# Kernel tuning notes

Measured on AMD Instinct MI355X. Metric: run time of the kernel, lower is better.

The kernel has to match this reference:

```python
import jax, jax.numpy as jnp
import numpy as np

N_MEL = 80; ARNN = 1024; ADIM = 128; EMB = 512; PRE = 256; DRNN = 1024; NF = 32; KS = 31
B = 32; NCTX = 512; T = 500
PAD = (KS - 1) // 2


def setup_inputs() -> dict:
    key = jax.random.key(0)
    ks = jax.random.split(key, 20)
    g = lambda k, shape: jax.random.normal(k, shape, dtype=jnp.float32) * 0.02
    return {
        "memory": jax.random.normal(ks[0], (B, NCTX, EMB), dtype=jnp.float32),
        "decoder_inputs": jax.random.normal(ks[1], (B, N_MEL, T), dtype=jnp.float32),
        "mask": jnp.zeros((B, NCTX), dtype=bool),
        "prenet_w1": g(ks[2], (PRE, N_MEL)),
        "prenet_w2": g(ks[3], (PRE, PRE)),
        "arnn_wih": g(ks[4], (4 * ARNN, PRE + EMB)),
        "arnn_whh": g(ks[5], (4 * ARNN, ARNN)),
        "arnn_bih": jnp.zeros((4 * ARNN,), jnp.float32),
        "arnn_bhh": jnp.zeros((4 * ARNN,), jnp.float32),
        "q_w": g(ks[6], (ADIM, ARNN)),
        "m_w": g(ks[7], (ADIM, EMB)),
        "loc_conv_w": g(ks[8], (NF, 2, KS)),
        "loc_w": g(ks[9], (ADIM, NF)),
        "v_w": g(ks[10], (ADIM,)),
        "drnn_wih": g(ks[11], (4 * DRNN, ARNN + EMB)),
        "drnn_whh": g(ks[12], (4 * DRNN, DRNN)),
        "drnn_bih": jnp.zeros((4 * DRNN,), jnp.float32),
        "drnn_bhh": jnp.zeros((4 * DRNN,), jnp.float32),
        "proj_w": g(ks[13], (N_MEL, DRNN + EMB)),
        "proj_b": jnp.zeros((N_MEL,), jnp.float32),
        "gate_w": g(ks[14], (1, DRNN + EMB)),
        "gate_b": jnp.zeros((1,), jnp.float32),
    }


def _lstm_cell(x, h, c, wih, whh, bih, bhh):
    # PyTorch LSTMCell gate order: i, f, g, o
    z = x @ wih.T + h @ whh.T + bih + bhh
    i, f, g, o = jnp.split(z, 4, axis=-1)
    c2 = jax.nn.sigmoid(f) * c + jax.nn.sigmoid(i) * jnp.tanh(g)
    h2 = jax.nn.sigmoid(o) * jnp.tanh(c2)
    return h2, c2


def reference(memory, decoder_inputs, mask,
              prenet_w1, prenet_w2,
              arnn_wih, arnn_whh, arnn_bih, arnn_bhh,
              q_w, m_w, loc_conv_w, loc_w, v_w,
              drnn_wih, drnn_whh, drnn_bih, drnn_bhh,
              proj_w, proj_b, gate_w, gate_b):
    b, n_ctx, emb = memory.shape
    n_mel, t_out = decoder_inputs.shape[1], decoder_inputs.shape[2]

    # (time, batch, n_mel) with a leading zero go-frame; PreNet (eval: no dropout)
    x = jnp.transpose(decoder_inputs, (2, 0, 1))
    x = jnp.concatenate([jnp.zeros((1, b, n_mel), x.dtype), x], axis=0)
    h = jax.nn.relu(x @ prenet_w1.T)
    h = jax.nn.relu(h @ prenet_w2.T)  # (T+1, B, PRE)
    inputs = h[:-1]  # T decoder steps

    proc_mem = memory @ m_w.T  # (B, n_ctx, ADIM)

    def step(carry, xin):
        ah, ac, dh, dc, aw, awc, actx = carry
        cell_in = jnp.concatenate([xin, actx], axis=-1)
        ah, ac = _lstm_cell(cell_in, ah, ac, arnn_wih, arnn_whh, arnn_bih, arnn_bhh)
        # location-sensitive attention
        aw_cat = jnp.stack([aw, awc], axis=1)  # (B, 2, n_ctx)
        loc = jax.lax.conv_general_dilated(
            aw_cat, loc_conv_w, window_strides=(1,), padding=[(PAD, PAD)],
            dimension_numbers=("NCH", "OIH", "NCH"))  # (B, NF, n_ctx)
        loc = jnp.transpose(loc, (0, 2, 1)) @ loc_w.T  # (B, n_ctx, ADIM)
        q = (ah @ q_w.T)[:, None, :]  # (B, 1, ADIM)
        e = jnp.tanh(q + proc_mem + loc) @ v_w  # (B, n_ctx)
        e = jnp.where(mask, -1e9, e)
        aw = jax.nn.softmax(e, axis=-1)
        actx = jnp.einsum("bn,bne->be", aw, memory)
        awc = awc + aw
        din = jnp.concatenate([ah, actx], axis=-1)
        dh, dc = _lstm_cell(din, dh, dc, drnn_wih, drnn_whh, drnn_bih, drnn_bhh)
        dhc = jnp.concatenate([dh, actx], axis=-1)
        mel = dhc @ proj_w.T + proj_b  # (B, n_mel)
        gate = dhc @ gate_w.T + gate_b  # (B, 1)
        return (ah, ac, dh, dc, aw, awc, actx), (mel, gate[:, 0])

    z32 = lambda *s: jnp.zeros(s, memory.dtype)
    carry0 = (z32(b, ARNN), z32(b, ARNN), z32(b, DRNN), z32(b, DRNN),
              z32(b, n_ctx), z32(b, n_ctx), z32(b, emb))
    _, (mels, gates) = jax.lax.scan(step, carry0, inputs)
    mel_out = jnp.transpose(mels, (1, 2, 0))   # (B, n_mel, T)
    gate_out = jnp.transpose(gates, (1, 0))    # (B, T)
    return mel_out, gate_out
```

## Files before the change

### kernel.cpp

```cpp
#include <hip/hip_runtime.h>

#define NBLK 256
#define NTHR 512

constexpr int kNMel = 80, kArnn = 1024, kAdim = 128, kEmb = 512, kPre = 256;
constexpr int kNF = 32, kKS = 31, kB = 32, kNctx = 512, kT = 500, kPad = 15;

constexpr int KT_A = 56;
constexpr int KT_D = 80;
constexpr int KT_ALL = KT_A + KT_D;

constexpr int OFF_PREB   = 0;
constexpr int OFF_PROCMB = OFF_PREB + kT * kB * kPre / 2;
constexpr int OFF_QWTB   = OFF_PROCMB + kB * kNctx * kAdim / 2;
constexpr int OFF_LWT    = OFF_QWTB + kAdim * kArnn / 2;
constexpr int OFF_STATE  = OFF_LWT + kAdim * 33;
constexpr int OFF_AHB    = OFF_STATE;
constexpr int OFF_DHB    = OFF_AHB + 2 * kB * kArnn / 2;
constexpr int OFF_DH     = OFF_DHB + 2 * kB * kArnn / 2;
constexpr int OFF_AC     = OFF_DH + 2 * kB * kArnn;
constexpr int OFF_DC     = OFF_AC + kB * kArnn;
constexpr int OFF_ACTX   = OFF_DC + kB * kArnn;
constexpr int OFF_AW     = OFF_ACTX + kB * kEmb;
constexpr int OFF_AWC    = OFF_AW + kB * kNctx;
constexpr int OFF_PAW    = OFF_AWC + kB * kNctx;
constexpr int OFF_NUM    = OFF_PAW + kB * kNctx;
constexpr int OFF_DEN    = OFF_NUM + 2 * kB * kEmb;
constexpr int OFF_END    = OFF_DEN + 2 * kB;
constexpr int STATE_SZ   = OFF_END - OFF_STATE;
constexpr int OFF_BAR    = OFF_END;
constexpr int BAR_LINES  = 266;
constexpr int OFF_PAN    = OFF_BAR + BAR_LINES * 32;
constexpr int PAN_SZ     = NBLK * KT_ALL * 256;
constexpr int OFF_GMB    = OFF_PAN + PAN_SZ;
constexpr int GMB_SZ     = kB * kNctx * kEmb / 2;

typedef __attribute__((ext_vector_type(4))) float fvec4;
typedef __attribute__((ext_vector_type(8))) short bh8_t;
typedef unsigned long long u64;
typedef unsigned short ushortt;

union U64u { u64 u; float2 f2; ushortt s[4]; };

union SMem {
  struct { ushortt xs[8][2][2048]; } x1;
  struct { float zra[4][2][64][4]; float zrd[4][2][64][4];
           float hb[2][32][4]; } x2;
  struct { float ahb_s[kArnn]; float vw_s[kAdim]; float psum[512]; float q_s[kAdim];
           float aw_s[96]; float awc_s[96]; float cw[kNF * 2 * kKS];
           float loc_s[64 * 33]; float p_s[64]; float lwt[kAdim * 33];
           float dhc[kArnn + kEmb]; float pprj[126];
           ushortt pm[64 * kAdim]; } b;
  struct { float x8[8][80]; float h1[8][256]; } p;
  struct { float mem_s[4][512]; } m;
};

__device__ __forceinline__ float sigf(float x) { return 1.0f / (1.0f + __expf(-x)); }
__device__ __forceinline__ float tanhfast(float x) { return 1.0f - 2.0f / (__expf(2.0f * x) + 1.0f); }

__device__ __forceinline__ ushortt bf16rn(float f) {
  unsigned u = __float_as_uint(f);
  unsigned r = (u + 0x7FFFu + ((u >> 16) & 1u)) >> 16;
  return (ushortt)r;
}
__device__ __forceinline__ float bf2f(ushortt v) {
  return __uint_as_float((unsigned)v << 16);
}

__device__ __forceinline__ u64 ald64(const void* p) {
  return __hip_atomic_load((const u64*)p, __ATOMIC_RELAXED, __HIP_MEMORY_SCOPE_AGENT);
}
__device__ __forceinline__ float alf(const float* p) {
  return __hip_atomic_load(p, __ATOMIC_RELAXED, __HIP_MEMORY_SCOPE_AGENT);
}
__device__ __forceinline__ void asf(float* p, float v) {
  __hip_atomic_store(p, v, __ATOMIC_RELAXED, __HIP_MEMORY_SCOPE_AGENT);
}
__device__ __forceinline__ void as64(void* p, u64 v) {
  __hip_atomic_store((u64*)p, v, __ATOMIC_RELAXED, __HIP_MEMORY_SCOPE_AGENT);
}
__device__ __forceinline__ unsigned alu(const unsigned* p) {
  return __hip_atomic_load(p, __ATOMIC_RELAXED, __HIP_MEMORY_SCOPE_AGENT);
}
__device__ __forceinline__ void asu(unsigned* p, unsigned v) {
  __hip_atomic_store(p, v, __ATOMIC_RELAXED, __HIP_MEMORY_SCOPE_AGENT);
}

__device__ __forceinline__ void gbar_full(unsigned* cnt, unsigned* gen, unsigned& genv) {
  __syncthreads();
  if (threadIdx.x == 0) {
    __threadfence();
    unsigned arrived = __hip_atomic_fetch_add(cnt, 1u, __ATOMIC_ACQ_REL, __HIP_MEMORY_SCOPE_AGENT) + 1u;
    if (arrived == (unsigned)NBLK) {
      __hip_atomic_store(cnt, 0u, __ATOMIC_RELAXED, __HIP_MEMORY_SCOPE_AGENT);
      __hip_atomic_fetch_add(gen, 1u, __ATOMIC_ACQ_REL, __HIP_MEMORY_SCOPE_AGENT);
    } else {
      while (__hip_atomic_load(gen, __ATOMIC_ACQUIRE, __HIP_MEMORY_SCOPE_AGENT) == genv) {
        __builtin_amdgcn_s_sleep(2);
      }
    }
    ++genv;
  }
  __syncthreads();
}

__device__ __forceinline__ void gbar_light(unsigned* bar, unsigned target, int bk, int tid) {
  asm volatile("s_waitcnt vmcnt(0) lgkmcnt(0)" ::: "memory");
  __syncthreads();
  if (bk == 0) {
    if (tid < 64) {
      if (tid == 0) {
        asm volatile("s_waitcnt vmcnt(0)" ::: "memory");
      }
      unsigned i1 = (unsigned)tid * 4 + 1, i2 = i1 + 1, i3 = i1 + 2;
      unsigned i0 = (unsigned)tid * 4;
      for (;;) {
        bool ok = true;
        if (i0 != 0) ok = ok && (alu(&bar[i0 * 32]) >= target);
        ok = ok && (alu(&bar[i1 * 32]) >= target);
        ok = ok && (alu(&bar[i2 * 32]) >= target);
        ok = ok && (alu(&bar[i3 * 32]) >= target);
        if (__all(ok)) break;
        __builtin_amdgcn_s_sleep(1);
      }
      if (tid < 8) asu(&bar[(256 + tid) * 32], target);
    }
  } else {
    if (tid == 0) {
      asm volatile("s_waitcnt vmcnt(0)" ::: "memory");
      asu(&bar[bk * 32], target);
      unsigned* wk = &bar[(256 + (bk & 7)) * 32];
      while (alu(wk) < target) __builtin_amdgcn_s_sleep(1);
    }
  }
  __syncthreads();
}

template<int LS, int W>
__device__ __forceinline__ void lstm_wave(
    const ushortt* __restrict__ s0, const ushortt* __restrict__ s2,
    const float* __restrict__ numq, const float* __restrict__ invden,
    const short* __restrict__ pan,
    int l, ushortt* xstg, fvec4& z0, fvec4& z1)
{
  constexpr int NC  = LS ? 10 : 7;
  constexpr int CB  = LS ? W * 640 : W * 448;
  constexpr int KT0 = LS ? W * 20 : W * 14;
  constexpr int BD0 = LS ? 1024 : 256;
  constexpr int BD1 = LS ? 1536 : 768;
  const int u8 = l & 15, rj = l >> 4;
  const int m = l & 15, kg = l >> 4;

  u64 L0[8], L1[8];
  bh8_t f00, f01, f10, f11;

  auto load = [&](int c, u64* L, bh8_t& f0, bh8_t& f1) {
    const int c0 = CB + c * 64;
    if (c0 >= BD0 && c0 < BD1) {
      const float* base = numq + (c0 - BD0) + u8 * 4;
      #pragma unroll
      for (int j = 0; j < 8; ++j) {
        int row = 4 * j + rj;
        const float* fp = base + (size_t)row * kEmb;
        U64u a, b2; a.u = ald64(fp); b2.u = ald64(fp + 2);
        float s = invden[row];
        U64u pk;
        pk.s[0] = bf16rn(a.f2.x * s);  pk.s[1] = bf16rn(a.f2.y * s);
        pk.s[2] = bf16rn(b2.f2.x * s); pk.s[3] = bf16rn(b2.f2.y * s);
        L[j] = pk.u;
      }
    } else {
      const ushortt* bsrc; int stride; bool coh;
      if (c0 < BD0) { bsrc = s0 + c0;       stride = (LS ? 1024 : 256); coh = (LS == 1); }
      else          { bsrc = s2 + c0 - BD1; stride = 1024;              coh = true; }
      #pragma unroll
      for (int j = 0; j < 8; ++j) {
        const ushortt* ap = bsrc + (size_t)(4 * j + rj) * stride + u8 * 4;
        L[j] = coh ? ald64(ap) : *reinterpret_cast<const u64*>(ap);
      }
    }
    f0 = *reinterpret_cast<const bh8_t*>(pan + (size_t)(KT0 + c * 2) * 512 + l * 8);
    f1 = *reinterpret_cast<const bh8_t*>(pan + (size_t)(KT0 + c * 2 + 1) * 512 + l * 8);
  };
  auto stash = [&](int buf, u64* L) {
    #pragma unroll
    for (int j = 0; j < 8; ++j) {
      int row = 4 * j + rj;
      int sw = u8 ^ ((row & 7) << 1);
      *reinterpret_cast<u64*>(xstg + buf * 2048 + row * 64 + sw * 4) = L[j];
    }
  };
  auto consume = [&](int buf, bh8_t f0, bh8_t f1) {
    #pragma unroll
    for (int kt = 0; kt < 2; ++kt) {
      int sw = (2 * (kt * 4 + kg)) ^ ((m & 7) << 1);
      bh8_t a0 = *reinterpret_cast<const bh8_t*>(xstg + buf * 2048 + m * 64 + sw * 4);
      bh8_t a1 = *reinterpret_cast<const bh8_t*>(xstg + buf * 2048 + (16 + m) * 64 + sw * 4);
      bh8_t f = kt ? f1 : f0;
      z0 = __builtin_amdgcn_mfma_f32_16x16x32_bf16(a0, f, z0, 0, 0, 0);
      z1 = __builtin_amdgcn_mfma_f32_16x16x32_bf16(a1, f, z1, 0, 0, 0);
    }
  };

  load(0, L0, f00, f01);
  #pragma unroll
  for (int c = 0; c < NC; c += 2) {
    stash(0, L0);
    if (c + 1 < NC) load(c + 1, L1, f10, f11);
    consume(0, f00, f01);
    if (c + 1 < NC) {
      stash(1, L1);
      if (c + 2 < NC) load(c + 2, L0, f00, f01);
      consume(1, f10, f11);
    }
  }
}

extern "C" __global__ void __launch_bounds__(NTHR, 1)
decoder_kernel(const float* __restrict__ gmem, const float* __restrict__ dec,
               const unsigned char* __restrict__ mask,
               const float* __restrict__ pw1, const float* __restrict__ pw2,
               const float* __restrict__ awih, const float* __restrict__ awhh,
               const float* __restrict__ abih, const float* __restrict__ abhh,
               const float* __restrict__ qw, const float* __restrict__ mw,
               const float* __restrict__ cvw, const float* __restrict__ locw,
               const float* __restrict__ vw,
               const float* __restrict__ dwih, const float* __restrict__ dwhh,
               const float* __restrict__ dbih, const float* __restrict__ dbhh,
               const float* __restrict__ pjw, const float* __restrict__ pjb,
               const float* __restrict__ gw, const float* __restrict__ gb,
               float* __restrict__ out, float* __restrict__ ws, int useg)
{
  __shared__ SMem sm;
  __shared__ float s_invden[32];
  const int bk = blockIdx.x, tid = threadIdx.x;
  unsigned genv_f = 0, bcnt = 0;
  unsigned* bar = reinterpret_cast<unsigned*>(ws + OFF_BAR);
  unsigned* cntF = &bar[264 * 32];
  unsigned* genF = &bar[265 * 32];

  ushortt* PREBu = reinterpret_cast<ushortt*>(ws + OFF_PREB);
  ushortt* PROCMBu = reinterpret_cast<ushortt*>(ws + OFF_PROCMB);
  ushortt* QWTBu = reinterpret_cast<ushortt*>(ws + OFF_QWTB);
  float* LWT = ws + OFF_LWT;
  ushortt* AHBu = reinterpret_cast<ushortt*>(ws + OFF_AHB);
  ushortt* DHBu = reinterpret_cast<ushortt*>(ws + OFF_DHB);
  float* DH = ws + OFF_DH;
  float* AC = ws + OFF_AC;
  float* DC = ws + OFF_DC;
  float* ACTX = ws + OFF_ACTX;
  float* AWp = ws + OFF_AW;
  float* AWC = ws + OFF_AWC;
  float* PAW = ws + OFF_PAW;
  float* NUM = ws + OFF_NUM;
  float* DEN = ws + OFF_DEN;
  short* PANS = reinterpret_cast<short*>(ws + OFF_PAN);
  ushortt* GMB = reinterpret_cast<ushortt*>(ws + OFF_GMB);

  for (int i = bk * NTHR + tid; i < STATE_SZ; i += NBLK * NTHR) (ws + OFF_STATE)[i] = 0.f;
  for (int i = bk * NTHR + tid; i < kAdim * kArnn; i += NBLK * NTHR)
    QWTBu[i] = bf16rn(qw[i]);
  for (int i = bk * NTHR + tid; i < kAdim * kNF; i += NBLK * NTHR) {
    int d = i >> 5, f = i & 31;
    LWT[d * 33 + f] = locw[i];
  }
  gbar_full(cntF, genF, genv_f);

  if (bk == 0 && tid < 2 * kB) asf(&DEN[tid], 1.0f);
  for (int it = 0; it < 16; ++it) {
    int task0 = bk * 64 + it * 4;
    for (int i = tid; i < 2048; i += NTHR) {
      int pr = i >> 9, h = i & 511;
      sm.m.mem_s[pr][h] = gmem[(size_t)(task0 + pr) * kEmb + h];
    }
    __syncthreads();
    {
      int pr = tid >> 7, d = tid & 127;
      const float* mwr = mw + d * kEmb;
      float acc = 0.f;
      for (int h = 0; h < kEmb; ++h) acc = fmaf(sm.m.mem_s[pr][h], mwr[h], acc);
      PROCMBu[(size_t)(task0 + pr) * kAdim + d] = bf16rn(acc);
    }
    if (useg) {
      for (int i = tid; i < 2048; i += NTHR) {
        int pr = i >> 9, h = i & 511;
        GMB[(size_t)(task0 + pr) * kEmb + h] = bf16rn(sm.m.mem_s[pr][h]);
      }
    }
    __syncthreads();
  }
  for (int g = bk; g < 2000; g += NBLK) {
    int t_idx = g >> 2;
    int b0 = (g & 3) * 8;
    if (t_idx == 0) {
      for (int i = tid; i < 8 * kPre; i += NTHR)
        PREBu[(size_t)(b0 + (i >> 8)) * kPre + (i & 255)] = 0;
      continue;
    }
    for (int i = tid; i < 640; i += NTHR) {
      int bb = i / 80, m2 = i % 80;
      sm.p.x8[bb][m2] = dec[((size_t)(b0 + bb) * kNMel + m2) * kT + (t_idx - 1)];
    }
    __syncthreads();
    {
      int u = tid & 255, rep = tid >> 8;
      float acc[4] = {0.f, 0.f, 0.f, 0.f};
      for (int m2 = 0; m2 < 80; ++m2) {
        float w = pw1[u * kNMel + m2];
        #pragma unroll
        for (int r = 0; r < 4; ++r) acc[r] = fmaf(w, sm.p.x8[rep * 4 + r][m2], acc[r]);
      }
      #pragma unroll
      for (int r = 0; r < 4; ++r) sm.p.h1[rep * 4 + r][u] = fmaxf(acc[r], 0.f);
    }
    __syncthreads();
    {
      int u = tid & 255, rep = tid >> 8;
      float acc[4] = {0.f, 0.f, 0.f, 0.f};
      for (int k = 0; k < kPre; ++k) {
        float w = pw2[u * kPre + k];
        #pragma unroll
        for (int r = 0; r < 4; ++r) acc[r] = fmaf(w, sm.p.h1[rep * 4 + r][k], acc[r]);
      }
      #pragma unroll
      for (int r = 0; r < 4; ++r)
        PREBu[((size_t)t_idx * kB + b0 + rep * 4 + r) * kPre + u] = bf16rn(fmaxf(acc[r], 0.f));
    }
    __syncthreads();
  }
  {
    const int UNITS = NBLK * KT_ALL * 64;
    for (int u = bk * NTHR + tid; u < UNITS; u += NBLK * NTHR) {
      int bkk = u / (KT_ALL * 64);
      int rem = u - bkk * (KT_ALL * 64);
      int kta = rem >> 6, l = rem & 63;
      int lstm = (kta >= KT_A);
      int kt = lstm ? kta - KT_A : kta;
      int n = l & 15, kg = l >> 4;
      int r = (n >> 2) * 1024 + bkk * 4 + (n & 3);
      bh8_t v;
      #pragma unroll
      for (int j = 0; j < 8; ++j) {
        int k = kt * 32 + kg * 8 + j;
        float wv;
        if (!lstm) wv = (k < 768) ? awih[(size_t)r * 768 + k] : awhh[(size_t)r * 1024 + (k - 768)];
        else       wv = (k < 1536) ? dwih[(size_t)r * 1536 + k] : dwhh[(size_t)r * 1024 + (k - 1536)];
        v[j] = (short)bf16rn(wv);
      }
      *reinterpret_cast<bh8_t*>(PANS + (size_t)u * 8) = v;
    }
  }
  gbar_full(cntF, genF, genv_f);

  for (int t = 0; t <= kT; ++t) {
    const int p = t & 1, q = p ^ 1;
    float* nump = NUM + p * kB * kEmb;
    const float* numq = NUM + q * kB * kEmb;

    if (tid < kB) s_invden[tid] = 1.0f / alf(DEN + q * kB + tid);
    __syncthreads();
    if (t > 0 && tid < 64) {
      int idx = bk * 64 + tid;
      int b2 = idx >> 9;
      float invd = s_invden[b2];
      float av = PAW[idx] * invd;
      asf(&AWp[idx], av);
      asf(&AWC[idx], alf(&AWC[idx]) + av);
      asf(&ACTX[idx], alf(&numq[idx]) * invd);
    }
    if (t < kT) {
      if (tid < 64) asf(&nump[bk * 64 + tid], 0.f);
      if (bk == 0 && tid < kB) asf(DEN + p * kB + tid, 0.f);
    }
    {
      const int w8 = tid >> 6, l = tid & 63;
      fvec4 z0 = {0.f, 0.f, 0.f, 0.f}, z1 = z0;
      const ushortt* AHBq_ = AHBu + q * kB * kArnn;
      const ushortt* DHBp_ = DHBu + p * kB * kArnn;
      const ushortt* preb_t = PREBu + (size_t)t * kB * kPre;
      ushortt* xst = &sm.x1.xs[w8][0][0];
      const short* panb = PANS + (size_t)bk * (KT_ALL * 512);
      const short* pand = panb + KT_A * 512;
      if (w8 < 4) {
        if (t < kT) {
          switch (w8) {
            case 0: lstm_wave<0,0>(preb_t, AHBq_, numq, s_invden, panb, l, xst, z0, z1); break;
            case 1: lstm_wave<0,1>(preb_t, AHBq_, numq, s_invden, panb, l, xst, z0, z1); break;
            case 2: lstm_wave<0,2>(preb_t, AHBq_, numq, s_invden, panb, l, xst, z0, z1); break;
            default: lstm_wave<0,3>(preb_t, AHBq_, numq, s_invden, panb, l, xst, z0, z1); break;
          }
        }
      } else {
        if (t > 0) {
          switch (w8) {
            case 4: lstm_wave<1,0>(AHBq_, DHBp_, numq, s_invden, pand, l, xst, z0, z1); break;
            case 5: lstm_wave<1,1>(AHBq_, DHBp_, numq, s_invden, pand, l, xst, z0, z1); break;
            case 6: lstm_wave<1,2>(AHBq_, DHBp_, numq, s_invden, pand, l, xst, z0, z1); break;
            default: lstm_wave<1,3>(AHBq_, DHBp_, numq, s_invden, pand, l, xst, z0, z1); break;
          }
        }
      }
      __syncthreads();
      if (w8 < 4) {
        *reinterpret_cast<fvec4*>(&sm.x2.zra[w8][0][l][0]) = z0;
        *reinterpret_cast<fvec4*>(&sm.x2.zra[w8][1][l][0]) = z1;
      } else {
        *reinterpret_cast<fvec4*>(&sm.x2.zrd[w8 - 4][0][l][0]) = z0;
        *reinterpret_cast<fvec4*>(&sm.x2.zrd[w8 - 4][1][l][0]) = z1;
      }
    }
    __syncthreads();
    if (tid < 256) {
      const int ls = tid >> 7, uu = (tid >> 5) & 3, b = tid & 31;
      const bool go = (ls == 0) ? (t < kT) : (t > 0);
      if (go) {
        const int mt = b >> 4, mm = b & 15;
        const int lane_base = (mm >> 2) * 16, rr = mm & 3;
        float zg[4];
        #pragma unroll
        for (int g = 0; g < 4; ++g) {
          int ln = lane_base + g * 4 + uu;
          float s;
          if (ls == 0)
            s = sm.x2.zra[0][mt][ln][rr] + sm.x2.zra[1][mt][ln][rr]
              + sm.x2.zra[2][mt][ln][rr] + sm.x2.zra[3][mt][ln][rr];
          else
            s = sm.x2.zrd[0][mt][ln][rr] + sm.x2.zrd[1][mt][ln][rr]
              + sm.x2.zrd[2][mt][ln][rr] + sm.x2.zrd[3][mt][ln][rr];
          int rg = g * 1024 + bk * 4 + uu;
          s += (ls ? dbih[rg] + dbhh[rg] : abih[rg] + abhh[rg]);
          zg[g] = s;
        }
        float* cst = ls ? DC : AC;
        const int idx = b * kArnn + bk * 4 + uu;
        float c = sigf(zg[1]) * cst[idx] + sigf(zg[0]) * tanhfast(zg[2]);
        cst[idx] = c;
        float h = sigf(zg[3]) * tanhfast(c);
        if (ls) asf(&DH[q * kB * kArnn + idx], h);
        sm.x2.hb[ls][b][uu] = h;
      }
    }
    __syncthreads();
    if (tid < 64) {
      int ls = tid >> 5, b = tid & 31;
      bool go2 = ls ? (t > 0) : (t < kT);
      if (go2) {
        U64u pk;
        #pragma unroll
        for (int j = 0; j < 4; ++j) pk.s[j] = bf16rn(sm.x2.hb[ls][b][j]);
        ushortt* dst = (ls ? (DHBu + q * kB * kArnn) : (AHBu + p * kB * kArnn)) + b * kArnn + bk * 4;
        as64(dst, pk.u);
      }
    }
    gbar_light(bar, ++bcnt, bk, tid);

    if (t < kT) {
      const int b = bk >> 3, sub = bk & 7, j0 = sub * 64;
      const int pbase = (sub == 0) ? 0 : 21 + (sub - 1) * 20;
      const int pcnt = (sub == 0) ? 21 : 20;
      const ushortt* AHBp_ = AHBu + p * kB * kArnn;
      if (tid < 256) {
        U64u v; v.u = ald64(AHBp_ + b * kArnn + tid * 4);
        #pragma unroll
        for (int j = 0; j < 4; ++j) sm.b.ahb_s[tid * 4 + j] = bf2f(v.s[j]);
      }
      for (int i = tid; i < 94; i += NTHR) {
        int jj = j0 - kPad + i;
        bool ok = (jj >= 0 && jj < kNctx);
        sm.b.aw_s[i] = ok ? alf(&AWp[b * kNctx + jj]) : 0.f;
        sm.b.awc_s[i] = ok ? alf(&AWC[b * kNctx + jj]) : 0.f;
      }
      for (int i = tid; i < kNF * 2 * kKS; i += NTHR) sm.b.cw[i] = cvw[i];
      for (int i = tid; i < kAdim * 33; i += NTHR) sm.b.lwt[i] = LWT[i];
      for (int i = tid; i < kAdim; i += NTHR) sm.b.vw_s[i] = vw[i];
      {
        const fvec4* src = reinterpret_cast<const fvec4*>(PROCMBu + (size_t)(b * kNctx + j0) * kAdim);
        fvec4* dst = reinterpret_cast<fvec4*>(sm.b.pm);
        for (int i = tid; i < 1024; i += NTHR) dst[i] = src[i];
      }
      if (sub < 4 && t > 0) {
        for (int i = tid; i < kArnn + kEmb; i += NTHR)
          sm.b.dhc[i] = (i < kArnn) ? alf(&DH[q * kB * kArnn + b * kArnn + i])
                                    : alf(&ACTX[b * kEmb + (i - kArnn)]);
      }
      __syncthreads();
      {
        int d = tid & 127, qr = tid >> 7;
        const ushortt* wq = QWTBu + (size_t)d * kArnn + qr * 256;
        const float* ahs = sm.b.ahb_s + qr * 256;
        float acc = 0.f;
        #pragma unroll 4
        for (int h8 = 0; h8 < 32; ++h8) {
          U64u a, c2;
          a.u = *reinterpret_cast<const u64*>(wq + h8 * 8);
          c2.u = *reinterpret_cast<const u64*>(wq + h8 * 8 + 4);
          #pragma unroll
          for (int j = 0; j < 4; ++j) acc = fmaf(bf2f(a.s[j]), ahs[h8 * 8 + j], acc);
          #pragma unroll
          for (int j = 0; j < 4; ++j) acc = fmaf(bf2f(c2.s[j]), ahs[h8 * 8 + 4 + j], acc);
        }
        sm.b.psum[tid] = acc;
      }
      __syncthreads();
      if (tid < kAdim)
        sm.b.q_s[tid] = sm.b.psum[tid] + sm.b.psum[128 + tid]
                      + sm.b.psum[256 + tid] + sm.b.psum[384 + tid];
      {
        int j = tid >> 3, f0 = (tid & 7) * 4;
        #pragma unroll
        for (int fi = 0; fi < 4; ++fi) {
          int f = f0 + fi;
          const float* w0 = &sm.b.cw[f * 62];
          float s = 0.f;
          for (int k = 0; k < kKS; ++k)
            s = fmaf(sm.b.aw_s[j + k], w0[k], fmaf(sm.b.awc_s[j + k], w0[31 + k], s));
          sm.b.loc_s[j * 33 + f] = s;
        }
      }
      if (sub < 4 && t > 0 && tid < pcnt * 6) {
        int ol = tid / 6, kc = tid % 6, og = pbase + ol;
        const float* row = (og < kNMel) ? pjw + (size_t)og * (kArnn + kEmb) : gw;
        const float* x = sm.b.dhc + kc * 256;
        const float* r2 = row + kc * 256;
        float acc = 0.f;
        for (int k = 0; k < 256; ++k) acc = fmaf(r2[k], x[k], acc);
        sm.b.pprj[tid] = acc;
      }
      __syncthreads();
      {
        int j = tid >> 3, grp = tid & 7, jj = j0 + j;
        float pe = 0.f;
        #pragma unroll 4
        for (int dd = 0; dd < 16; ++dd) {
          int d = grp + 8 * dd;
          float l2 = 0.f;
          const float* ls2 = &sm.b.loc_s[j * 33];
          const float* lw2 = &sm.b.lwt[d * 33];
          #pragma unroll 8
          for (int f = 0; f < kNF; ++f) l2 = fmaf(ls2[f], lw2[f], l2);
          float x = sm.b.q_s[d] + bf2f(sm.b.pm[j * kAdim + d]) + l2;
          pe = fmaf(sm.b.vw_s[d], tanhfast(x), pe);
        }
        pe += __shfl_xor(pe, 1);
        pe += __shfl_xor(pe, 2);
        pe += __shfl_xor(pe, 4);
        if (grp == 0) {
          float pv = mask[b * kNctx + jj] ? 0.f : __expf(pe);
          sm.b.p_s[j] = pv;
          PAW[b * kNctx + jj] = pv;
        }
      }
      if (sub < 4 && t > 0 && tid < pcnt) {
        int og = pbase + tid;
        float val = (og < kNMel) ? pjb[og] : gb[0];
        #pragma unroll
        for (int kc = 0; kc < 6; ++kc) val += sm.b.pprj[tid * 6 + kc];
        if (og < kNMel) out[((size_t)b * kNMel + og) * kT + (t - 1)] = val;
        else out[(size_t)kB * kNMel * kT + b * kT + (t - 1)] = val;
      }
      __syncthreads();
      if (tid < 64) {
        float v = sm.b.p_s[tid];
        #pragma unroll
        for (int o = 1; o < 64; o <<= 1) v += __shfl_xor(v, o);
        if (tid == 0) atomicAdd(DEN + p * kB + b, v);
      }
      if (useg) {
        const ushortt* memb = GMB + (size_t)(b * kNctx + j0) * kEmb + tid;
        float a0 = 0.f, a1 = 0.f, a2 = 0.f, a3 = 0.f;
        #pragma unroll 4
        for (int jj2 = 0; jj2 < 64; jj2 += 4) {
          a0 = fmaf(sm.b.p_s[jj2],     bf2f(memb[(size_t)jj2 * kEmb]), a0);
          a1 = fmaf(sm.b.p_s[jj2 + 1], bf2f(memb[(size_t)(jj2 + 1) * kEmb]), a1);
          a2 = fmaf(sm.b.p_s[jj2 + 2], bf2f(memb[(size_t)(jj2 + 2) * kEmb]), a2);
          a3 = fmaf(sm.b.p_s[jj2 + 3], bf2f(memb[(size_t)(jj2 + 3) * kEmb]), a3);
        }
        atomicAdd(&nump[b * kEmb + tid], (a0 + a1) + (a2 + a3));
      } else {
        const float* memb = gmem + (size_t)(b * kNctx + j0) * kEmb + tid;
        float a0 = 0.f, a1 = 0.f;
        #pragma unroll 8
        for (int jj2 = 0; jj2 < 64; jj2 += 2) {
          a0 = fmaf(sm.b.p_s[jj2], memb[(size_t)jj2 * kEmb], a0);
          a1 = fmaf(sm.b.p_s[jj2 + 1], memb[(size_t)(jj2 + 1) * kEmb], a1);
        }
        atomicAdd(&nump[b * kEmb + tid], a0 + a1);
      }
      gbar_light(bar, ++bcnt, bk, tid);
    }
  }

  if (bk < kB) {
    const int b = bk;
    for (int i = tid; i < kArnn + kEmb; i += NTHR)
      sm.b.dhc[i] = (i < kArnn) ? alf(&DH[1 * kB * kArnn + b * kArnn + i])
                                : alf(&ACTX[b * kEmb + (i - kArnn)]);
    __syncthreads();
    if (tid < 486) {
      int ol = tid / 6, kc = tid % 6;
      const float* row = (ol < kNMel) ? pjw + (size_t)ol * (kArnn + kEmb) : gw;
      const float* x = sm.b.dhc + kc * 256;
      const float* r2 = row + kc * 256;
      float acc = 0.f;
      for (int k = 0; k < 256; ++k) acc = fmaf(r2[k], x[k], acc);
      sm.b.psum[tid] = acc;
    }
    __syncthreads();
    if (tid < 81) {
      float val = (tid < kNMel) ? pjb[tid] : gb[0];
      #pragma unroll
      for (int kc = 0; kc < 6; ++kc) val += sm.b.psum[tid * 6 + kc];
      if (tid < kNMel) out[((size_t)b * kNMel + tid) * kT + (kT - 1)] = val;
      else out[(size_t)kB * kNMel * kT + b * kT + (kT - 1)] = val;
    }
  }
}

extern "C" void kernel_launch(void* const* d_in, const int* in_sizes, int n_in,
                              void* d_out, int out_size, void* d_ws, size_t ws_size,
                              hipStream_t stream) {
  const float* gmem = (const float*)d_in[0];
  const float* dec = (const float*)d_in[1];
  const unsigned char* mask = (const unsigned char*)d_in[2];
  const float* pw1 = (const float*)d_in[3];
  const float* pw2 = (const float*)d_in[4];
  const float* awih = (const float*)d_in[5];
  const float* awhh = (const float*)d_in[6];
  const float* abih = (const float*)d_in[7];
  const float* abhh = (const float*)d_in[8];
  const float* qw = (const float*)d_in[9];
  const float* mw = (const float*)d_in[10];
  const float* cvw = (const float*)d_in[11];
  const float* locw = (const float*)d_in[12];
  const float* vw = (const float*)d_in[13];
  const float* dwih = (const float*)d_in[14];
  const float* dwhh = (const float*)d_in[15];
  const float* dbih = (const float*)d_in[16];
  const float* dbhh = (const float*)d_in[17];
  const float* pjw = (const float*)d_in[18];
  const float* pjb = (const float*)d_in[19];
  const float* gw = (const float*)d_in[20];
  const float* gb = (const float*)d_in[21];
  float* out = (float*)d_out;
  float* ws = (float*)d_ws;

  int useg = (ws_size >= (size_t)(OFF_GMB + GMB_SZ) * sizeof(float)) ? 1 : 0;

  hipMemsetAsync((char*)d_ws + (size_t)OFF_BAR * sizeof(float), 0,
                 (size_t)BAR_LINES * 128, stream);
  hipLaunchKernelGGL(decoder_kernel, dim3(NBLK), dim3(NTHR), 0, stream,
                     gmem, dec, mask, pw1, pw2, awih, awhh, abih, abhh, qw, mw,
                     cvw, locw, vw, dwih, dwhh, dbih, dbhh, pjw, pjb, gw, gb,
                     out, ws, useg);
}
```

Baseline: 38.91 ms.

## Double block size to 1024 threads and split LSTM waves by M-half

Raises threads per block from 512 to 1024 and splits each LSTM GEMM slice across two waves, with each wave owning one 16-row half of the batch and a single MFMA accumulator instead of two. The query projection reduction and the attention-context accumulation over memory rows are also split across the extra threads, and some phases are gated to the first 512 threads. The intent is more latency hiding and shorter per-wave serial chains within each persistent step. In exchange it adds register pressure limits (launch bounds changed to 1024,4), duplicated fragment loads of the weight panels, and more atomics to the context accumulator.

```diff
diff --git a/kernel.cpp b/kernel.cpp
--- a/kernel.cpp
+++ b/kernel.cpp
@@ -1,7 +1,7 @@
 #include <hip/hip_runtime.h>
 
 #define NBLK 256
-#define NTHR 512
+#define NTHR 1024
 
 constexpr int kNMel = 80, kArnn = 1024, kAdim = 128, kEmb = 512, kPre = 256;
 constexpr int kNF = 32, kKS = 31, kB = 32, kNctx = 512, kT = 500, kPad = 15;
@@ -43,10 +43,10 @@
 union U64u { u64 u; float2 f2; ushortt s[4]; };
 
 union SMem {
-  struct { ushortt xs[8][2][2048]; } x1;
+  struct { ushortt xs[16][2048]; } x1;
   struct { float zra[4][2][64][4]; float zrd[4][2][64][4];
            float hb[2][32][4]; } x2;
-  struct { float ahb_s[kArnn]; float vw_s[kAdim]; float psum[512]; float q_s[kAdim];
+  struct { float ahb_s[kArnn]; float vw_s[kAdim]; float psum[1024]; float q_s[kAdim];
            float aw_s[96]; float awc_s[96]; float cw[kNF * 2 * kKS];
            float loc_s[64 * 33]; float p_s[64]; float lwt[kAdim * 33];
            float dhc[kArnn + kEmb]; float pprj[126];
@@ -109,11 +109,8 @@
   __syncthreads();
   if (bk == 0) {
     if (tid < 64) {
-      if (tid == 0) {
-        asm volatile("s_waitcnt vmcnt(0)" ::: "memory");
-      }
-      unsigned i1 = (unsigned)tid * 4 + 1, i2 = i1 + 1, i3 = i1 + 2;
-      unsigned i0 = (unsigned)tid * 4;
+      if (tid == 0) asm volatile("s_waitcnt vmcnt(0)" ::: "memory");
+      unsigned i0 = (unsigned)tid * 4, i1 = i0 + 1, i2 = i0 + 2, i3 = i0 + 3;
       for (;;) {
         bool ok = true;
         if (i0 != 0) ok = ok && (alu(&bar[i0 * 32]) >= target);
@@ -136,22 +133,22 @@
   __syncthreads();
 }
 
-template<int LS, int W>
+template<int LS, int SL, int MH>
 __device__ __forceinline__ void lstm_wave(
     const ushortt* __restrict__ s0, const ushortt* __restrict__ s2,
     const float* __restrict__ numq, const float* __restrict__ invden,
     const short* __restrict__ pan,
-    int l, ushortt* xstg, fvec4& z0, fvec4& z1)
+    int l, ushortt* xs, fvec4& z)
 {
   constexpr int NC  = LS ? 10 : 7;
-  constexpr int CB  = LS ? W * 640 : W * 448;
-  constexpr int KT0 = LS ? W * 20 : W * 14;
+  constexpr int CB  = LS ? SL * 640 : SL * 448;
+  constexpr int KT0 = LS ? SL * 20 : SL * 14;
   constexpr int BD0 = LS ? 1024 : 256;
   constexpr int BD1 = LS ? 1536 : 768;
   const int u8 = l & 15, rj = l >> 4;
   const int m = l & 15, kg = l >> 4;
 
-  u64 L0[8], L1[8];
+  u64 L0[4], L1[4];
   bh8_t f00, f01, f10, f11;
 
   auto load = [&](int c, u64* L, bh8_t& f0, bh8_t& f1) {
@@ -159,11 +156,11 @@
     if (c0 >= BD0 && c0 < BD1) {
       const float* base = numq + (c0 - BD0) + u8 * 4;
       #pragma unroll
-      for (int j = 0; j < 8; ++j) {
-        int row = 4 * j + rj;
-        const float* fp = base + (size_t)row * kEmb;
+      for (int j = 0; j < 4; ++j) {
+        int lr = 4 * j + rj;
+        const float* fp = base + (size_t)(MH * 16 + lr) * kEmb;
         U64u a, b2; a.u = ald64(fp); b2.u = ald64(fp + 2);
-        float s = invden[row];
+        float s = invden[MH * 16 + lr];
         U64u pk;
         pk.s[0] = bf16rn(a.f2.x * s);  pk.s[1] = bf16rn(a.f2.y * s);
         pk.s[2] = bf16rn(b2.f2.x * s); pk.s[3] = bf16rn(b2.f2.y * s);
@@ -174,8 +171,8 @@
       if (c0 < BD0) { bsrc = s0 + c0;       stride = (LS ? 1024 : 256); coh = (LS == 1); }
       else          { bsrc = s2 + c0 - BD1; stride = 1024;              coh = true; }
       #pragma unroll
-      for (int j = 0; j < 8; ++j) {
-        const ushortt* ap = bsrc + (size_t)(4 * j + rj) * stride + u8 * 4;
+      for (int j = 0; j < 4; ++j) {
+        const ushortt* ap = bsrc + (size_t)(MH * 16 + 4 * j + rj) * stride + u8 * 4;
         L[j] = coh ? ald64(ap) : *reinterpret_cast<const u64*>(ap);
       }
     }
@@ -184,21 +181,18 @@
   };
   auto stash = [&](int buf, u64* L) {
     #pragma unroll
-    for (int j = 0; j < 8; ++j) {
-      int row = 4 * j + rj;
-      int sw = u8 ^ ((row & 7) << 1);
-      *reinterpret_cast<u64*>(xstg + buf * 2048 + row * 64 + sw * 4) = L[j];
+    for (int j = 0; j < 4; ++j) {
+      int lr = 4 * j + rj;
+      int sw = u8 ^ ((lr & 7) << 1);
+      *reinterpret_cast<u64*>(xs + buf * 1024 + lr * 64 + sw * 4) = L[j];
     }
   };
   auto consume = [&](int buf, bh8_t f0, bh8_t f1) {
     #pragma unroll
     for (int kt = 0; kt < 2; ++kt) {
       int sw = (2 * (kt * 4 + kg)) ^ ((m & 7) << 1);
-      bh8_t a0 = *reinterpret_cast<const bh8_t*>(xstg + buf * 2048 + m * 64 + sw * 4);
-      bh8_t a1 = *reinterpret_cast<const bh8_t*>(xstg + buf * 2048 + (16 + m) * 64 + sw * 4);
-      bh8_t f = kt ? f1 : f0;
-      z0 = __builtin_amdgcn_mfma_f32_16x16x32_bf16(a0, f, z0, 0, 0, 0);
-      z1 = __builtin_amdgcn_mfma_f32_16x16x32_bf16(a1, f, z1, 0, 0, 0);
+      bh8_t a = *reinterpret_cast<const bh8_t*>(xs + buf * 1024 + m * 64 + sw * 4);
+      z = __builtin_amdgcn_mfma_f32_16x16x32_bf16(a, kt ? f1 : f0, z, 0, 0, 0);
     }
   };
 
@@ -216,7 +210,7 @@
   }
 }
 
-extern "C" __global__ void __launch_bounds__(NTHR, 1)
+extern "C" __global__ void __launch_bounds__(NTHR, 4)
 decoder_kernel(const float* __restrict__ gmem, const float* __restrict__ dec,
                const unsigned char* __restrict__ mask,
                const float* __restrict__ pw1, const float* __restrict__ pw2,
@@ -274,7 +268,7 @@
       sm.m.mem_s[pr][h] = gmem[(size_t)(task0 + pr) * kEmb + h];
     }
     __syncthreads();
-    {
+    if (tid < 512) {
       int pr = tid >> 7, d = tid & 127;
       const float* mwr = mw + d * kEmb;
       float acc = 0.f;
@@ -302,7 +296,7 @@
       sm.p.x8[bb][m2] = dec[((size_t)(b0 + bb) * kNMel + m2) * kT + (t_idx - 1)];
     }
     __syncthreads();
-    {
+    if (tid < 512) {
       int u = tid & 255, rep = tid >> 8;
       float acc[4] = {0.f, 0.f, 0.f, 0.f};
       for (int m2 = 0; m2 < 80; ++m2) {
@@ -314,7 +308,7 @@
       for (int r = 0; r < 4; ++r) sm.p.h1[rep * 4 + r][u] = fmaxf(acc[r], 0.f);
     }
     __syncthreads();
-    {
+    if (tid < 512) {
       int u = tid & 255, rep = tid >> 8;
       float acc[4] = {0.f, 0.f, 0.f, 0.f};
       for (int k = 0; k < kPre; ++k) {
@@ -373,41 +367,45 @@
       if (bk == 0 && tid < kB) asf(DEN + p * kB + tid, 0.f);
     }
     {
-      const int w8 = tid >> 6, l = tid & 63;
-      fvec4 z0 = {0.f, 0.f, 0.f, 0.f}, z1 = z0;
+      const int wid = tid >> 6, l = tid & 63;
+      fvec4 z = {0.f, 0.f, 0.f, 0.f};
       const ushortt* AHBq_ = AHBu + q * kB * kArnn;
       const ushortt* DHBp_ = DHBu + p * kB * kArnn;
       const ushortt* preb_t = PREBu + (size_t)t * kB * kPre;
-      ushortt* xst = &sm.x1.xs[w8][0][0];
+      ushortt* xs = &sm.x1.xs[wid][0];
       const short* panb = PANS + (size_t)bk * (KT_ALL * 512);
       const short* pand = panb + KT_A * 512;
-      if (w8 < 4) {
+      if (wid < 8) {
         if (t < kT) {
-          switch (w8) {
-            case 0: lstm_wave<0,0>(preb_t, AHBq_, numq, s_invden, panb, l, xst, z0, z1); break;
-            case 1: lstm_wave<0,1>(preb_t, AHBq_, numq, s_invden, panb, l, xst, z0, z1); break;
-            case 2: lstm_wave<0,2>(preb_t, AHBq_, numq, s_invden, panb, l, xst, z0, z1); break;
-            default: lstm_wave<0,3>(preb_t, AHBq_, numq, s_invden, panb, l, xst, z0, z1); break;
+          switch (wid) {
+            case 0: lstm_wave<0,0,0>(preb_t, AHBq_, numq, s_invden, panb, l, xs, z); break;
+            case 1: lstm_wave<0,0,1>(preb_t, AHBq_, numq, s_invden, panb, l, xs, z); break;
+            case 2: lstm_wave<0,1,0>(preb_t, AHBq_, numq, s_invden, panb, l, xs, z); break;
+            case 3: lstm_wave<0,1,1>(preb_t, AHBq_, numq, s_invden, panb, l, xs, z); break;
+            case 4: lstm_wave<0,2,0>(preb_t, AHBq_, numq, s_invden, panb, l, xs, z); break;
+            case 5: lstm_wave<0,2,1>(preb_t, AHBq_, numq, s_invden, panb, l, xs, z); break;
+            case 6: lstm_wave<0,3,0>(preb_t, AHBq_, numq, s_invden, panb, l, xs, z); break;
+            default: lstm_wave<0,3,1>(preb_t, AHBq_, numq, s_invden, panb, l, xs, z); break;
           }
         }
       } else {
         if (t > 0) {
-          switch (w8) {
-            case 4: lstm_wave<1,0>(AHBq_, DHBp_, numq, s_invden, pand, l, xst, z0, z1); break;
-            case 5: lstm_wave<1,1>(AHBq_, DHBp_, numq, s_invden, pand, l, xst, z0, z1); break;
-            case 6: lstm_wave<1,2>(AHBq_, DHBp_, numq, s_invden, pand, l, xst, z0, z1); break;
-            default: lstm_wave<1,3>(AHBq_, DHBp_, numq, s_invden, pand, l, xst, z0, z1); break;
+          switch (wid) {
+            case 8:  lstm_wave<1,0,0>(AHBq_, DHBp_, numq, s_invden, pand, l, xs, z); break;
+            case 9:  lstm_wave<1,0,1>(AHBq_, DHBp_, numq, s_invden, pand, l, xs, z); break;
+            case 10: lstm_wave<1,1,0>(AHBq_, DHBp_, numq, s_invden, pand, l, xs, z); break;
+            case 11: lstm_wave<1,1,1>(AHBq_, DHBp_, numq, s_invden, pand, l, xs, z); break;
+            case 12: lstm_wave<1,2,0>(AHBq_, DHBp_, numq, s_invden, pand, l, xs, z); break;
+            case 13: lstm_wave<1,2,1>(AHBq_, DHBp_, numq, s_invden, pand, l, xs, z); break;
+            case 14: lstm_wave<1,3,0>(AHBq_, DHBp_, numq, s_invden, pand, l, xs, z); break;
+            default: lstm_wave<1,3,1>(AHBq_, DHBp_, numq, s_invden, pand, l, xs, z); break;
           }
         }
       }
       __syncthreads();
-      if (w8 < 4) {
-        *reinterpret_cast<fvec4*>(&sm.x2.zra[w8][0][l][0]) = z0;
-        *reinterpret_cast<fvec4*>(&sm.x2.zra[w8][1][l][0]) = z1;
-      } else {
-        *reinterpret_cast<fvec4*>(&sm.x2.zrd[w8 - 4][0][l][0]) = z0;
-        *reinterpret_cast<fvec4*>(&sm.x2.zrd[w8 - 4][1][l][0]) = z1;
-      }
+      const int sl = (wid & 7) >> 1, mh = wid & 1;
+      if (wid < 8) *reinterpret_cast<fvec4*>(&sm.x2.zra[sl][mh][l][0]) = z;
+      else         *reinterpret_cast<fvec4*>(&sm.x2.zrd[sl][mh][l][0]) = z;
     }
     __syncthreads();
     if (tid < 256) {
@@ -486,11 +484,11 @@
       __syncthreads();
       {
         int d = tid & 127, qr = tid >> 7;
-        const ushortt* wq = QWTBu + (size_t)d * kArnn + qr * 256;
-        const float* ahs = sm.b.ahb_s + qr * 256;
+        const ushortt* wq = QWTBu + (size_t)d * kArnn + qr * 128;
+        const float* ahs = sm.b.ahb_s + qr * 128;
         float acc = 0.f;
         #pragma unroll 4
-        for (int h8 = 0; h8 < 32; ++h8) {
+        for (int h8 = 0; h8 < 16; ++h8) {
           U64u a, c2;
           a.u = *reinterpret_cast<const u64*>(wq + h8 * 8);
           c2.u = *reinterpret_cast<const u64*>(wq + h8 * 8 + 4);
@@ -502,10 +500,13 @@
         sm.b.psum[tid] = acc;
       }
       __syncthreads();
-      if (tid < kAdim)
-        sm.b.q_s[tid] = sm.b.psum[tid] + sm.b.psum[128 + tid]
-                      + sm.b.psum[256 + tid] + sm.b.psum[384 + tid];
-      {
+      if (tid < kAdim) {
+        float s = 0.f;
+        #pragma unroll
+        for (int k = 0; k < 8; ++k) s += sm.b.psum[tid + 128 * k];
+        sm.b.q_s[tid] = s;
+      }
+      if (tid < 512) {
         int j = tid >> 3, f0 = (tid & 7) * 4;
         #pragma unroll
         for (int fi = 0; fi < 4; ++fi) {
@@ -527,7 +528,7 @@
         sm.b.pprj[tid] = acc;
       }
       __syncthreads();
-      {
+      if (tid < 512) {
         int j = tid >> 3, grp = tid & 7, jj = j0 + j;
         float pe = 0.f;
         #pragma unroll 4
@@ -565,26 +566,30 @@
         for (int o = 1; o < 64; o <<= 1) v += __shfl_xor(v, o);
         if (tid == 0) atomicAdd(DEN + p * kB + b, v);
       }
-      if (useg) {
-        const ushortt* memb = GMB + (size_t)(b * kNctx + j0) * kEmb + tid;
-        float a0 = 0.f, a1 = 0.f, a2 = 0.f, a3 = 0.f;
-        #pragma unroll 4
-        for (int jj2 = 0; jj2 < 64; jj2 += 4) {
-          a0 = fmaf(sm.b.p_s[jj2],     bf2f(memb[(size_t)jj2 * kEmb]), a0);
-          a1 = fmaf(sm.b.p_s[jj2 + 1], bf2f(memb[(size_t)(jj2 + 1) * kEmb]), a1);
-          a2 = fmaf(sm.b.p_s[jj2 + 2], bf2f(memb[(size_t)(jj2 + 2) * kEmb]), a2);
-          a3 = fmaf(sm.b.p_s[jj2 + 3], bf2f(memb[(size_t)(jj2 + 3) * kEmb]), a3);
-        }
-        atomicAdd(&nump[b * kEmb + tid], (a0 + a1) + (a2 + a3));
-      } else {
-        const float* memb = gmem + (size_t)(b * kNctx + j0) * kEmb + tid;
-        float a0 = 0.f, a1 = 0.f;
-        #pragma unroll 8
-        for (int jj2 = 0; jj2 < 64; jj2 += 2) {
-          a0 = fmaf(sm.b.p_s[jj2], memb[(size_t)jj2 * kEmb], a0);
-          a1 = fmaf(sm.b.p_s[jj2 + 1], memb[(size_t)(jj2 + 1) * kEmb], a1);
-        }
-        atomicAdd(&nump[b * kEmb + tid], a0 + a1);
+      {
+        int col = tid & 511, half = tid >> 9;
+        int jbase = half * 32;
+        if (useg) {
+          const ushortt* memb = GMB + (size_t)(b * kNctx + j0 + jbase) * kEmb + col;
+          float a0 = 0.f, a1 = 0.f, a2 = 0.f, a3 = 0.f;
+          #pragma unroll 4
+          for (int jj2 = 0; jj2 < 32; jj2 += 4) {
+            a0 = fmaf(sm.b.p_s[jbase + jj2],     bf2f(memb[(size_t)jj2 * kEmb]), a0);
+            a1 = fmaf(sm.b.p_s[jbase + jj2 + 1], bf2f(memb[(size_t)(jj2 + 1) * kEmb]), a1);
+            a2 = fmaf(sm.b.p_s[jbase + jj2 + 2], bf2f(memb[(size_t)(jj2 + 2) * kEmb]), a2);
+            a3 = fmaf(sm.b.p_s[jbase + jj2 + 3], bf2f(memb[(size_t)(jj2 + 3) * kEmb]), a3);
+          }
+          atomicAdd(&nump[b * kEmb + col], (a0 + a1) + (a2 + a3));
+        } else {
+          const float* memb = gmem + (size_t)(b * kNctx + j0 + jbase) * kEmb + col;
+          float a0 = 0.f, a1 = 0.f;
+          #pragma unroll 8
+          for (int jj2 = 0; jj2 < 32; jj2 += 2) {
+            a0 = fmaf(sm.b.p_s[jbase + jj2], memb[(size_t)jj2 * kEmb], a0);
+            a1 = fmaf(sm.b.p_s[jbase + jj2 + 1], memb[(size_t)(jj2 + 1) * kEmb], a1);
+          }
+          atomicAdd(&nump[b * kEmb + col], a0 + a1);
+        }
       }
       gbar_light(bar, ++bcnt, bk, tid);
     }
```

Measured after the change: 40.14 ms. 1.03x slower.
